# Optimization experiments

Measured on AMD Instinct MI355X. Metric: run time of the kernel, lower is better.

## Reference

```python
import jax, jax.numpy as jnp
import numpy as np

F = 128          # feature_size
N = 512          # num_vertices (batch_size fixed to 1 by the original indexing)
C = 32 * 7 * 7 * 7   # 10976, f2 channel dim
G = 13           # f2 spatial grid (indices = (v+1)*6 in [0,12])
EPS = 1e-5


def _block(x, W1, b1, W2, b2, g, be, m, v):
    # Linear -> ELU -> Linear -> ELU -> Dropout(eval=id) -> BatchNorm1d(eval)
    h = jax.nn.elu(x @ W1 + b1)
    h = jax.nn.elu(h @ W2 + b2)
    return (h - m) * (g * jax.lax.rsqrt(v + EPS)) + be


def setup_inputs() -> dict:
    key = jax.random.key(0)
    ks = iter(jax.random.split(key, 80))

    def nrm(sh, s):
        return jax.random.normal(next(ks), sh, jnp.float32) * s

    def lin(i, o):
        return nrm((i, o), 1.0 / np.sqrt(i)), nrm((o,), 0.01)

    def bn():
        g = 1.0 + nrm((F,), 0.05)
        be = nrm((F,), 0.05)
        m = nrm((F,), 0.1)
        v = jax.random.uniform(next(ks), (F,), jnp.float32) + 0.5
        return g, be, m, v

    d = {}
    d['vertices'] = jax.random.uniform(next(ks), (1, N, 3), jnp.float32) * 2.0 - 1.0
    d['f2'] = nrm((1, G, G, G, C), 0.1)
    ii = jnp.arange(N, dtype=jnp.int32)
    d['v1s_idx'] = jnp.repeat(ii, N)   # edge k=(i,j): i = k//N
    d['v2s_idx'] = jnp.tile(ii, N)     #               j = k%N
    d['adj'] = (jax.random.uniform(next(ks), (N, N)) < 0.05).astype(jnp.float32)

    for p, (i, o) in [('mv', (3, F)), ('mf', (C, F)), ('s1', (2 * F, F)),
                      ('s2', (F, F)), ('s3', (2 * F, F))]:
        W1, b1 = lin(i, o)
        W2, b2 = lin(F, F)
        g, be, m, v = bn()
        d.update({p + '_W1': W1, p + '_b1': b1, p + '_W2': W2, p + '_b2': b2,
                  p + '_g': g, p + '_be': be, p + '_m': m, p + '_v': v})
    W3, b3 = lin(F, 2)
    d['s3_W3'], d['s3_b3'] = W3, b3
    return d


def _forward(vertices, f2, adj,
             mv_W1, mv_b1, mv_W2, mv_b2, mv_g, mv_be, mv_m, mv_v,
             mf_W1, mf_b1, mf_W2, mf_b2, mf_g, mf_be, mf_m, mf_v,
             s1_W1, s1_b1, s1_W2, s1_b2, s1_g, s1_be, s1_m, s1_v,
             s2_W1, s2_b1, s2_W2, s2_b2, s2_g, s2_be, s2_m, s2_v,
             s3_W1, s3_b1, s3_W2, s3_b2, s3_g, s3_be, s3_m, s3_v, s3_W3, s3_b3,
             v1s_idx, v2s_idx):
    b, n, _ = vertices.shape
    flat = vertices.reshape(-1, 3)                        # (B*N, 3)
    idx = ((flat + 1.0) * 6.0).astype(jnp.int32)          # grid indices in [0,12]
    f2e = f2[0, idx[:, 0], idx[:, 1], idx[:, 2], :]       # gather: (B*N, C)
    vf = _block(flat, mv_W1, mv_b1, mv_W2, mv_b2, mv_g, mv_be, mv_m, mv_v)
    ff = _block(f2e, mf_W1, mf_b1, mf_W2, mf_b2, mf_g, mf_be, mf_m, mf_v)
    vert = jnp.concatenate([vf, ff], -1).reshape(b, n, 2 * F)  # (B, N, 2F)

    # stage1: NodeToEdge (endpoint combine) -> MLP block over all N^2 edges
    e1 = vert[:, v1s_idx] + vert[:, v2s_idx]              # (B, N*N, 2F)
    s1 = _block(e1, s1_W1, s1_b1, s1_W2, s1_b2, s1_g, s1_be, s1_m, s1_v)  # (B, E, F)

    # stage2: EdgeToNode (adjacency-masked sum) -> MLP -> NodeToEdge
    nodes = jnp.einsum('bijf,ij->bif', s1.reshape(b, n, n, F), adj)  # (B, N, F)
    n2 = _block(nodes, s2_W1, s2_b1, s2_W2, s2_b2, s2_g, s2_be, s2_m, s2_v)
    s2 = n2[:, v1s_idx] + n2[:, v2s_idx]                  # (B, E, F)

    cat = jnp.concatenate([s1, s2], -1).reshape(b * n * n, 2 * F)
    h = _block(cat, s3_W1, s3_b1, s3_W2, s3_b2, s3_g, s3_be, s3_m, s3_v)
    return (h @ s3_W3 + s3_b3).reshape(b, n, n, 2)


def reference(vertices, f2, v1s_idx, v2s_idx, adj,
              mv_W1, mv_b1, mv_W2, mv_b2, mv_g, mv_be, mv_m, mv_v,
              mf_W1, mf_b1, mf_W2, mf_b2, mf_g, mf_be, mf_m, mf_v,
              s1_W1, s1_b1, s1_W2, s1_b2, s1_g, s1_be, s1_m, s1_v,
              s2_W1, s2_b1, s2_W2, s2_b2, s2_g, s2_be, s2_m, s2_v,
              s3_W1, s3_b1, s3_W2, s3_b2, s3_g, s3_be, s3_m, s3_v, s3_W3, s3_b3):
    return _forward(vertices, f2, adj,
                    mv_W1, mv_b1, mv_W2, mv_b2, mv_g, mv_be, mv_m, mv_v,
                    mf_W1, mf_b1, mf_W2, mf_b2, mf_g, mf_be, mf_m, mf_v,
                    s1_W1, s1_b1, s1_W2, s1_b2, s1_g, s1_be, s1_m, s1_v,
                    s2_W1, s2_b1, s2_W2, s2_b2, s2_g, s2_be, s2_m, s2_v,
                    s3_W1, s3_b1, s3_W2, s3_b2, s3_g, s3_be, s3_m, s3_v, s3_W3, s3_b3,
                    v1s_idx, v2s_idx)
```

## Files before the change

### kernel.cpp

```cpp
#include <hip/hip_runtime.h>
#include <hip/hip_bf16.h>


#define F    128
#define NV   512
#define CCC  10976
#define EPSV 1e-5f

typedef __attribute__((ext_vector_type(8)))  short        short8;
typedef __attribute__((ext_vector_type(4)))  float        f32x4;
typedef __attribute__((ext_vector_type(4)))  float        flt4;
typedef __attribute__((ext_vector_type(4)))  unsigned int u32x4;

union Frag { u32x4 q; short8 s; unsigned int d[4]; unsigned short u[8]; };

__device__ __forceinline__ unsigned short f2bf(float x){
  union { float f; unsigned int u; } c; c.f = x;
  unsigned int r = c.u + 0x7FFFu + ((c.u >> 16) & 1u);
  return (unsigned short)(r >> 16);
}
__device__ __forceinline__ unsigned int pkbf(float a, float b){
  union { __hip_bfloat162 h; unsigned int u; } cv;
  cv.h = __float22bfloat162_rn(make_float2(a, b));
  return cv.u;
}
__device__ __forceinline__ float eluf(float x){
  return x > 0.f ? x : (__expf(x) - 1.f);
}
__device__ __forceinline__ f32x4 mfma16(short8 a, short8 b, f32x4 c){
  return __builtin_amdgcn_mfma_f32_16x16x32_bf16(a, b, c, 0, 0, 0);
}

#define WS_U      0u
#define WS_FFPRE  262144u
#define WS_NODES  524288u
#define WS_WPERM  786432u
#define WS_ADJS   1048576u
#define WS_CNT    1050624u
#define WS_PJ     1052672u
#define WS_VEC    1183744u
#define WS_W2FS1  1188864u
#define WS_W1AFS3 1221632u
#define WS_W2FS3  1254400u
#define WS_W3F    1287168u
#define WS_MFW1F  1291264u
#define WS_END    4101120u
#define WS_PART   4101120u
#define WS_PART_END 8295424u


__global__ __launch_bounds__(256) void k_prep(
    const float* s1W2, const float* s3W1, const float* s3W2, const float* s3W3,
    const float* s1g, const float* s1be, const float* s1m, const float* s1v,
    const float* s3g, const float* s3be, const float* s3m, const float* s3v,
    const float* s1b2, const float* s3b2,
    unsigned short* w2fs1, unsigned short* w1afs3, unsigned short* w2fs3,
    unsigned short* w3f, float* vec, float* zeroreg)
{
  int t = blockIdx.x * 256 + threadIdx.x;
  if (t < 49152){
    int T = t >> 14, tt = t & 16383;
    int e = tt & 7, lane = (tt >> 3) & 63, grp = tt >> 9;
    int slot = (grp >> 3) * 32 + ((lane >> 4) & 3) * 8 + e;
    int col  = (grp & 7) * 16 + (lane & 15);
    float val;
    unsigned short* dst;
    if (T == 0){ dst = w2fs1; val = s1W2[slot * F + col]; }
    else {
      int kf = (slot & 7) * 16 + (slot >> 3);
      if (T == 1){
        float sc1 = s1g[kf] * rsqrtf(s1v[kf] + EPSV);
        dst = w1afs3; val = sc1 * s3W1[kf * F + col];
      } else {
        dst = w2fs3; val = s3W2[kf * F + col];
      }
    }
    dst[tt] = f2bf(val);
    return;
  }
  t -= 49152;
  if (t < 2048){
    int e = t & 7, lane = (t >> 3) & 63, ks = t >> 9;
    int slot = ks * 32 + ((lane >> 4) & 3) * 8 + e;
    int kf = (slot & 7) * 16 + (slot >> 3);
    int n = lane & 15;
    float sc3 = s3g[kf] * rsqrtf(s3v[kf] + EPSV);
    w3f[t] = f2bf(n < 2 ? sc3 * s3W3[kf * 2 + n] : 0.f);
    return;
  }
  t -= 2048;
  if (t < 1024){
    int f = t & 127, which = t >> 7;
    int s = (f & 15) * 8 + (f >> 4);
    switch (which){
      case 0: vec[512 + s] = s1b2[f]; break;
      case 1: vec[640 + s] = s3b2[f]; break;
      case 2: vec[768 + f] = s1g[f] * rsqrtf(s1v[f] + EPSV); break;
      case 3: vec[896 + f] = s1be[f] - s1m[f] * (s1g[f] * rsqrtf(s1v[f] + EPSV)); break;
      case 4: {
        float a = 0.f;
        for (int k = 0; k < F; ++k){
          float sc = s1g[k] * rsqrtf(s1v[k] + EPSV);
          a = fmaf(s1be[k] - s1m[k] * sc, s3W1[k * F + f], a);
        }
        vec[1024 + f] = a;
      } break;
      case 5: if (f < 16){
        float a = 0.f;
        if (f < 2){
          for (int k = 0; k < F; ++k){
            float sc = s3g[k] * rsqrtf(s3v[k] + EPSV);
            a = fmaf(s3be[k] - s3m[k] * sc, s3W3[k * 2 + f], a);
          }
        }
        vec[1152 + f] = a;
      } break;
      default: break;
    }
    return;
  }
  t -= 1024;
  if (t < 65536) zeroreg[t] = 0.f;
}

__global__ __launch_bounds__(256) void k_prepf(
    const float* __restrict__ mfW1, unsigned short* __restrict__ mfw1f)
{
  __shared__ float sm[32 * 132];
  int tid = threadIdx.x, ksg = blockIdx.x;
  const float* src = mfW1 + ksg * 32 * F;
  #pragma unroll
  for (int p = 0; p < 4; ++p){
    int g4 = tid + p * 256;
    int row = g4 >> 5, col = (g4 & 31) * 4;
    flt4 v = *(const flt4*)(src + row * F + col);
    *(flt4*)(sm + row * 132 + col) = v;
  }
  __syncthreads();
  unsigned int* dst = (unsigned int*)mfw1f + ksg * 2048;
  #pragma unroll
  for (int q2 = 0; q2 < 8; ++q2){
    int o = (tid * 8 + q2) * 2;
    int nt = o >> 9, lane = (o >> 3) & 63, e = o & 7;
    int k = (lane >> 4) * 8 + e;
    int n = nt * 16 + (lane & 15);
    dst[tid * 8 + q2] = pkbf(sm[k * 132 + n], sm[(k + 1) * 132 + n]);
  }
}

__global__ __launch_bounds__(256) void k_adj(
    const float* __restrict__ adj, unsigned short* __restrict__ pj,
    int* __restrict__ cntI, float* __restrict__ cntF)
{
  __shared__ unsigned long long msk[8];
  int i = blockIdx.x, tid = threadIdx.x, wv = tid >> 6, ln = tid & 63;
  bool p0 = adj[i * NV + tid] != 0.f;
  bool p1 = adj[i * NV + 256 + tid] != 0.f;
  unsigned long long m0 = __ballot(p0);
  unsigned long long m1 = __ballot(p1);
  if (ln == 0){ msk[wv] = m0; msk[4 + wv] = m1; }
  __syncthreads();
  int base0 = 0, base1 = 0, tot = 0;
  #pragma unroll
  for (int g = 0; g < 8; ++g){
    int c = __popcll(msk[g]);
    if (g < wv) base0 += c;
    if (g < 4 + wv) base1 += c;
    tot += c;
  }
  unsigned long long below = (1ull << ln) - 1ull;
  if (p0){
    int r = base0 + __popcll(m0 & below);
    if (r < 128) pj[i * 128 + r] = (unsigned short)tid;
  }
  if (p1){
    int r = base1 + __popcll(m1 & below);
    if (r < 128) pj[i * 128 + r] = (unsigned short)(256 + tid);
  }
  if (tid == 0){ cntI[i] = tot > 128 ? 128 : tot; cntF[i] = (float)tot; }
}

__global__ __launch_bounds__(256) void k_ff1(
    const float* __restrict__ verts, const float* __restrict__ f2,
    const unsigned short* __restrict__ mfw1f, float* __restrict__ ffpre,
    float* __restrict__ partials, int use_parts)
{
  int tid = threadIdx.x, w = tid >> 6, l = tid & 63, g = l >> 4, mm = l & 15;
  int mb = blockIdx.x & 7, kc = blockIdx.x >> 3;
  int v = mb * 64 + w * 16 + mm;
  float x0 = verts[v * 3 + 0], x1 = verts[v * 3 + 1], x2 = verts[v * 3 + 2];
  int i0 = (int)((x0 + 1.f) * 6.f), i1 = (int)((x1 + 1.f) * 6.f), i2 = (int)((x2 + 1.f) * 6.f);
  int base = ((i0 * 13 + i1) * 13 + i2) * CCC;

  f32x4 zero = {0.f, 0.f, 0.f, 0.f};
  f32x4 acc[8];
  #pragma unroll
  for (int nt = 0; nt < 8; ++nt) acc[nt] = zero;

  const u32x4* bt = (const u32x4*)mfw1f;
  for (int kk = 0; kk < 22; ++kk){
    int ksg = kc * 22 + kk;
    if (ksg >= 343) break;
    const float* ap = f2 + base + ksg * 32 + g * 8;
    flt4 a0 = *(const flt4*)ap;
    flt4 a1 = *(const flt4*)(ap + 4);
    Frag a;
    a.d[0] = pkbf(a0.x, a0.y); a.d[1] = pkbf(a0.z, a0.w);
    a.d[2] = pkbf(a1.x, a1.y); a.d[3] = pkbf(a1.z, a1.w);
    #pragma unroll
    for (int nt = 0; nt < 8; ++nt){
      Frag b; b.q = bt[(ksg * 8 + nt) * 64 + l];
      acc[nt] = mfma16(a.s, b.s, acc[nt]);
    }
  }
  if (use_parts){
    #pragma unroll
    for (int nt = 0; nt < 8; ++nt){
      int n = nt * 16 + mm;
      #pragma unroll
      for (int r = 0; r < 4; ++r)
        partials[(kc * NV + mb * 64 + w * 16 + g * 4 + r) * F + n] = acc[nt][r];
    }
  } else {
    #pragma unroll
    for (int nt = 0; nt < 8; ++nt){
      int n = nt * 16 + mm;
      #pragma unroll
      for (int r = 0; r < 4; ++r)
        atomicAdd(&ffpre[(mb * 64 + w * 16 + g * 4 + r) * F + n], acc[nt][r]);
    }
  }
}

__global__ __launch_bounds__(128) void k_vert(
    const float* __restrict__ verts, const float* __restrict__ ffpre,
    const float* __restrict__ partials, int use_parts,
    const float* mvW1, const float* mvb1, const float* mvW2, const float* mvb2,
    const float* mvg, const float* mvbe, const float* mvm, const float* mvv,
    const float* mfb1, const float* mfW2, const float* mfb2,
    const float* mfg, const float* mfbe, const float* mfm, const float* mfv,
    const float* s1W1, const float* s1b1, float* __restrict__ uP)
{
  __shared__ float hv[F], hf[F], vf[F], ff[F];
  int f = threadIdx.x, v = blockIdx.x;
  float x0 = verts[v * 3], x1 = verts[v * 3 + 1], x2 = verts[v * 3 + 2];
  hv[f] = eluf(mvb1[f] + x0 * mvW1[f] + x1 * mvW1[F + f] + x2 * mvW1[2 * F + f]);
  float fp;
  if (use_parts){
    fp = 0.f;
    for (int kc = 0; kc < 16; ++kc) fp += partials[(kc * NV + v) * F + f];
  } else {
    fp = ffpre[v * F + f];
  }
  hf[f] = eluf(fp + mfb1[f]);
  __syncthreads();
  float sv = mvb2[f], sf = mfb2[f];
  for (int k = 0; k < F; ++k){
    sv = fmaf(hv[k], mvW2[k * F + f], sv);
    sf = fmaf(hf[k], mfW2[k * F + f], sf);
  }
  vf[f] = (eluf(sv) - mvm[f]) * (mvg[f] * rsqrtf(mvv[f] + EPSV)) + mvbe[f];
  ff[f] = (eluf(sf) - mfm[f]) * (mfg[f] * rsqrtf(mfv[f] + EPSV)) + mfbe[f];
  __syncthreads();
  float u = 0.5f * s1b1[f];
  for (int k = 0; k < F; ++k){
    u = fmaf(vf[k], s1W1[k * F + f], u);
    u = fmaf(ff[k], s1W1[(128 + k) * F + f], u);
  }
  uP[v * F + f] = u;
}

__global__ __launch_bounds__(256) void k_pass1s(
    const float* __restrict__ uP, const unsigned short* __restrict__ w2fs1,
    const float* __restrict__ vec, const unsigned short* __restrict__ pj,
    const int* __restrict__ cntA, float* __restrict__ nodes)
{
  __shared__ u32x4 Wb[2048];
  __shared__ float ci[F], nblk[F];
  int tid = threadIdx.x, i = blockIdx.x;
  int cnt = cntA[i];
  { const u32x4* ws_ = (const u32x4*)w2fs1;
    #pragma unroll
    for (int ii = 0; ii < 8; ++ii) Wb[tid + 256 * ii] = ws_[tid + 256 * ii]; }
  if (tid < F){ ci[tid] = uP[i * F + tid]; nblk[tid] = 0.f; }
  __syncthreads();

  int w = tid >> 6, l = tid & 63, g = l >> 4, mm = l & 15;
  float b2v[8];
  *(flt4*)&b2v[0] = *(const flt4*)(vec + 512 + mm * 8);
  *(flt4*)&b2v[4] = *(const flt4*)(vec + 516 + mm * 8);

  for (int t = 0; t * 64 < cnt; ++t){
    int row = t * 64 + w * 16 + mm;
    int j = (row < cnt) ? (int)pj[i * 128 + row] : 0;
    f32x4 acc[8];
    #pragma unroll
    for (int nt = 0; nt < 8; ++nt){ float b = b2v[nt]; acc[nt] = (f32x4){b, b, b, b}; }
    #pragma unroll
    for (int ks = 0; ks < 4; ++ks){
      int kb = ks * 32 + g * 8;
      flt4 ua = *(const flt4*)(uP + j * F + kb);
      flt4 ub = *(const flt4*)(uP + j * F + kb + 4);
      flt4 c0 = *(const flt4*)&ci[kb];
      flt4 c1 = *(const flt4*)&ci[kb + 4];
      Frag a;
      a.d[0] = pkbf(eluf(ua.x + c0.x), eluf(ua.y + c0.y));
      a.d[1] = pkbf(eluf(ua.z + c0.z), eluf(ua.w + c0.w));
      a.d[2] = pkbf(eluf(ub.x + c1.x), eluf(ub.y + c1.y));
      a.d[3] = pkbf(eluf(ub.z + c1.z), eluf(ub.w + c1.w));
      #pragma unroll
      for (int nt = 0; nt < 8; ++nt){
        Frag b; b.q = Wb[(ks * 8 + nt) * 64 + l];
        acc[nt] = mfma16(a.s, b.s, acc[nt]);
      }
    }
    int rbase = t * 64 + w * 16 + g * 4;
    float mk[4];
    #pragma unroll
    for (int r = 0; r < 4; ++r) mk[r] = (rbase + r < cnt) ? 1.f : 0.f;
    #pragma unroll
    for (int nt = 0; nt < 8; ++nt){
      float s = mk[0] * eluf(acc[nt][0]);
      s = fmaf(mk[1], eluf(acc[nt][1]), s);
      s = fmaf(mk[2], eluf(acc[nt][2]), s);
      s = fmaf(mk[3], eluf(acc[nt][3]), s);
      s += __shfl_xor(s, 16, 64);
      s += __shfl_xor(s, 32, 64);
      if (l < 16) atomicAdd(&nblk[nt * 16 + mm], s);
    }
  }
  __syncthreads();
  if (tid < F) nodes[i * F + tid] = nblk[tid];
}

__global__ __launch_bounds__(128) void k_mid(
    const float* __restrict__ nodes, const float* __restrict__ cntF,
    const float* __restrict__ vec,
    const float* s2W1, const float* s2b1, const float* s2W2, const float* s2b2,
    const float* s2g, const float* s2be, const float* s2m, const float* s2v,
    const float* s3W1, const float* s3b1, float* __restrict__ wPp)
{
  __shared__ float a[F], b[F];
  int f = threadIdx.x, r = blockIdx.x;
  a[f] = vec[768 + f] * nodes[r * F + f] + vec[896 + f] * cntF[r];
  __syncthreads();
  float s = s2b1[f];
  for (int k = 0; k < F; ++k) s = fmaf(a[k], s2W1[k * F + f], s);
  b[f] = eluf(s);
  __syncthreads();
  float s2 = s2b2[f];
  for (int k = 0; k < F; ++k) s2 = fmaf(b[k], s2W2[k * F + f], s2);
  float n2 = (eluf(s2) - s2m[f]) * (s2g[f] * rsqrtf(s2v[f] + EPSV)) + s2be[f];
  __syncthreads();
  a[f] = n2;
  __syncthreads();
  float wv = 0.5f * (s3b1[f] + vec[1024 + f]);
  for (int k = 0; k < F; ++k) wv = fmaf(a[k], s3W1[(128 + k) * F + f], wv);
  wPp[r * F + ((f & 15) * 8 + (f >> 4))] = wv;
}

__global__ __launch_bounds__(512, 4) void k_pass3(
    const float* __restrict__ uP, const float* __restrict__ wPp,
    const unsigned short* __restrict__ w2fs1, const unsigned short* __restrict__ w1afs3,
    const unsigned short* __restrict__ w2fs3, const unsigned short* __restrict__ w3f,
    const float* __restrict__ vec, const float* __restrict__ s3b3,
    float* __restrict__ out)
{
  __shared__ u32x4 Wb[2048];
  __shared__ __align__(16) char Hb[32768];
  __shared__ float ci[F];
  int tid = threadIdx.x, bid = blockIdx.x;
  int band, idx;
  if (bid < 512)      { band = 0; idx = bid; }
  else if (bid < 896) { band = 1; idx = bid - 512; }
  else if (bid < 1152){ band = 2; idx = bid - 896; }
  else                { band = 3; idx = bid - 1152; }
  int tpb = 4 - band;
  int i  = band * 128 + idx / tpb;
  int j0 = (band + idx % tpb) * 128;

  int w = tid >> 6, l = tid & 63, g = l >> 4, mm = l & 15;
  char* hb = Hb + w * 4096;

  { const u32x4* ws_ = (const u32x4*)w2fs1;
    #pragma unroll
    for (int ii = 0; ii < 4; ++ii) Wb[tid + 512 * ii] = ws_[tid + 512 * ii]; }
  if (tid < F) ci[tid] = uP[i * F + tid];
  __syncthreads();

  int j = j0 + w * 16 + mm;
  f32x4 acc[8];
  {
    float b2v[8];
    *(flt4*)&b2v[0] = *(const flt4*)(vec + 512 + mm * 8);
    *(flt4*)&b2v[4] = *(const flt4*)(vec + 516 + mm * 8);
    #pragma unroll
    for (int nt = 0; nt < 8; ++nt){ float b = b2v[nt]; acc[nt] = (f32x4){b, b, b, b}; }
  }
  #pragma unroll
  for (int ks = 0; ks < 4; ++ks){
    int kb = ks * 32 + g * 8;
    flt4 ua = *(const flt4*)(uP + j * F + kb);
    flt4 ub = *(const flt4*)(uP + j * F + kb + 4);
    flt4 c0 = *(const flt4*)&ci[kb];
    flt4 c1 = *(const flt4*)&ci[kb + 4];
    Frag a;
    a.d[0] = pkbf(eluf(ua.x + c0.x), eluf(ua.y + c0.y));
    a.d[1] = pkbf(eluf(ua.z + c0.z), eluf(ua.w + c0.w));
    a.d[2] = pkbf(eluf(ub.x + c1.x), eluf(ub.y + c1.y));
    a.d[3] = pkbf(eluf(ub.z + c1.z), eluf(ub.w + c1.w));
    #pragma unroll
    for (int nt = 0; nt < 8; ++nt){
      Frag b; b.q = Wb[(ks * 8 + nt) * 64 + l];
      acc[nt] = mfma16(a.s, b.s, acc[nt]);
    }
  }
  #pragma unroll
  for (int r = 0; r < 4; ++r){
    int row = g * 4 + r;
    u32x4 wd;
    #pragma unroll
    for (int q = 0; q < 4; ++q)
      wd[q] = pkbf(eluf(acc[2*q][r]), eluf(acc[2*q+1][r]));
    *(u32x4*)(hb + row * 256 + ((mm * 16) ^ ((row & 7) << 4))) = wd;
  }
  __syncthreads();
  { const u32x4* ws_ = (const u32x4*)w1afs3;
    #pragma unroll
    for (int ii = 0; ii < 4; ++ii) Wb[tid + 512 * ii] = ws_[tid + 512 * ii]; }
  __syncthreads();

  {
    float wiv[8];
    *(flt4*)&wiv[0] = *(const flt4*)(wPp + i * F + mm * 8);
    *(flt4*)&wiv[4] = *(const flt4*)(wPp + i * F + mm * 8 + 4);
    #pragma unroll
    for (int nt = 0; nt < 8; ++nt){ float b = wiv[nt]; acc[nt] = (f32x4){b, b, b, b}; }
  }
  {
    int sx = (mm & 7) << 4;
    #pragma unroll
    for (int ks = 0; ks < 4; ++ks){
      Frag a; a.q = *(const u32x4*)(hb + mm * 256 + ((ks * 64 + g * 16) ^ sx));
      #pragma unroll
      for (int nt = 0; nt < 8; ++nt){
        Frag b; b.q = Wb[(ks * 8 + nt) * 64 + l];
        acc[nt] = mfma16(a.s, b.s, acc[nt]);
      }
    }
  }
  #pragma unroll
  for (int r = 0; r < 4; ++r){
    int row = g * 4 + r;
    int jj = j0 + w * 16 + row;
    float wjv[8];
    *(flt4*)&wjv[0] = *(const flt4*)(wPp + jj * F + mm * 8);
    *(flt4*)&wjv[4] = *(const flt4*)(wPp + jj * F + mm * 8 + 4);
    u32x4 wd;
    #pragma unroll
    for (int q = 0; q < 4; ++q)
      wd[q] = pkbf(eluf(acc[2*q][r] + wjv[2*q]), eluf(acc[2*q+1][r] + wjv[2*q+1]));
    *(u32x4*)(hb + row * 256 + ((mm * 16) ^ ((row & 7) << 4))) = wd;
  }
  __syncthreads();
  { const u32x4* ws_ = (const u32x4*)w2fs3;
    #pragma unroll
    for (int ii = 0; ii < 4; ++ii) Wb[tid + 512 * ii] = ws_[tid + 512 * ii]; }
  __syncthreads();

  {
    float b2v[8];
    *(flt4*)&b2v[0] = *(const flt4*)(vec + 640 + mm * 8);
    *(flt4*)&b2v[4] = *(const flt4*)(vec + 644 + mm * 8);
    #pragma unroll
    for (int nt = 0; nt < 8; ++nt){ float b = b2v[nt]; acc[nt] = (f32x4){b, b, b, b}; }
  }
  {
    int sx = (mm & 7) << 4;
    #pragma unroll
    for (int ks = 0; ks < 4; ++ks){
      Frag a; a.q = *(const u32x4*)(hb + mm * 256 + ((ks * 64 + g * 16) ^ sx));
      #pragma unroll
      for (int nt = 0; nt < 8; ++nt){
        Frag b; b.q = Wb[(ks * 8 + nt) * 64 + l];
        acc[nt] = mfma16(a.s, b.s, acc[nt]);
      }
    }
  }
  #pragma unroll
  for (int r = 0; r < 4; ++r){
    int row = g * 4 + r;
    u32x4 wd;
    #pragma unroll
    for (int q = 0; q < 4; ++q)
      wd[q] = pkbf(eluf(acc[2*q][r]), eluf(acc[2*q+1][r]));
    *(u32x4*)(hb + row * 256 + ((mm * 16) ^ ((row & 7) << 4))) = wd;
  }

  float bb = (mm < 2) ? (s3b3[mm] + vec[1152 + mm]) : 0.f;
  f32x4 acc4 = {bb, bb, bb, bb};
  {
    const u32x4* w3q = (const u32x4*)w3f;
    int sx = (mm & 7) << 4;
    #pragma unroll
    for (int ks = 0; ks < 4; ++ks){
      Frag a; a.q = *(const u32x4*)(hb + mm * 256 + ((ks * 64 + g * 16) ^ sx));
      Frag b; b.q = w3q[ks * 64 + l];
      acc4 = mfma16(a.s, b.s, acc4);
    }
  }
  if (mm < 2){
    #pragma unroll
    for (int r = 0; r < 4; ++r){
      int jr = j0 + w * 16 + g * 4 + r;
      if (jr >= i){
        float val = acc4[r];
        out[(i * NV + jr) * 2 + mm] = val;
        out[(jr * NV + i) * 2 + mm] = val;
      }
    }
  }
}

extern "C" void kernel_launch(void* const* d_in, const int* in_sizes, int n_in,
                              void* d_out, int out_size, void* d_ws, size_t ws_size,
                              hipStream_t stream)
{
  (void)in_sizes; (void)n_in; (void)out_size;
  const float* vertices = (const float*)d_in[0];
  const float* f2   = (const float*)d_in[1];
  const float* adj  = (const float*)d_in[4];
  const float* mvW1 = (const float*)d_in[5];
  const float* mvb1 = (const float*)d_in[6];
  const float* mvW2 = (const float*)d_in[7];
  const float* mvb2 = (const float*)d_in[8];
  const float* mvg  = (const float*)d_in[9];
  const float* mvbe = (const float*)d_in[10];
  const float* mvm  = (const float*)d_in[11];
  const float* mvv  = (const float*)d_in[12];
  const float* mfW1 = (const float*)d_in[13];
  const float* mfb1 = (const float*)d_in[14];
  const float* mfW2 = (const float*)d_in[15];
  const float* mfb2 = (const float*)d_in[16];
  const float* mfg  = (const float*)d_in[17];
  const float* mfbe = (const float*)d_in[18];
  const float* mfm  = (const float*)d_in[19];
  const float* mfv  = (const float*)d_in[20];
  const float* s1W1 = (const float*)d_in[21];
  const float* s1b1 = (const float*)d_in[22];
  const float* s1W2 = (const float*)d_in[23];
  const float* s1b2 = (const float*)d_in[24];
  const float* s1g  = (const float*)d_in[25];
  const float* s1be = (const float*)d_in[26];
  const float* s1m  = (const float*)d_in[27];
  const float* s1v  = (const float*)d_in[28];
  const float* s2W1 = (const float*)d_in[29];
  const float* s2b1 = (const float*)d_in[30];
  const float* s2W2 = (const float*)d_in[31];
  const float* s2b2 = (const float*)d_in[32];
  const float* s2g  = (const float*)d_in[33];
  const float* s2be = (const float*)d_in[34];
  const float* s2m  = (const float*)d_in[35];
  const float* s2v  = (const float*)d_in[36];
  const float* s3W1 = (const float*)d_in[37];
  const float* s3b1 = (const float*)d_in[38];
  const float* s3W2 = (const float*)d_in[39];
  const float* s3b2 = (const float*)d_in[40];
  const float* s3g  = (const float*)d_in[41];
  const float* s3be = (const float*)d_in[42];
  const float* s3m  = (const float*)d_in[43];
  const float* s3v  = (const float*)d_in[44];
  const float* s3W3 = (const float*)d_in[45];
  const float* s3b3 = (const float*)d_in[46];

  char* ws = (char*)d_ws;
  float* uP    = (float*)(ws + WS_U);
  float* ffpre = (float*)(ws + WS_FFPRE);
  float* nodes = (float*)(ws + WS_NODES);
  float* wPp   = (float*)(ws + WS_WPERM);
  float* cntF  = (float*)(ws + WS_ADJS);
  int*   cntI  = (int*)(ws + WS_CNT);
  unsigned short* pj = (unsigned short*)(ws + WS_PJ);
  float* vec   = (float*)(ws + WS_VEC);
  unsigned short* w2fs1  = (unsigned short*)(ws + WS_W2FS1);
  unsigned short* w1afs3 = (unsigned short*)(ws + WS_W1AFS3);
  unsigned short* w2fs3  = (unsigned short*)(ws + WS_W2FS3);
  unsigned short* w3f    = (unsigned short*)(ws + WS_W3F);
  unsigned short* mfw1f  = (unsigned short*)(ws + WS_MFW1F);
  float* parts = (float*)(ws + WS_PART);
  int use_parts = (ws_size >= (size_t)WS_PART_END) ? 1 : 0;

  k_prep<<<460, 256, 0, stream>>>(s1W2, s3W1, s3W2, s3W3,
      s1g, s1be, s1m, s1v, s3g, s3be, s3m, s3v, s1b2, s3b2,
      w2fs1, w1afs3, w2fs3, w3f, vec, ffpre);
  k_prepf<<<343, 256, 0, stream>>>(mfW1, mfw1f);
  k_adj<<<512, 256, 0, stream>>>(adj, pj, cntI, cntF);
  k_ff1<<<128, 256, 0, stream>>>(vertices, f2, mfw1f, ffpre, parts, use_parts);
  k_vert<<<512, 128, 0, stream>>>(vertices, ffpre, parts, use_parts,
      mvW1, mvb1, mvW2, mvb2, mvg, mvbe, mvm, mvv,
      mfb1, mfW2, mfb2, mfg, mfbe, mfm, mfv,
      s1W1, s1b1, uP);
  k_pass1s<<<512, 256, 0, stream>>>(uP, w2fs1, vec, pj, cntI, nodes);
  k_mid<<<512, 128, 0, stream>>>(nodes, cntF, vec,
      s2W1, s2b1, s2W2, s2b2, s2g, s2be, s2m, s2v, s3W1, s3b1, wPp);
  k_pass3<<<1280, 512, 0, stream>>>(uP, wPp, w2fs1, w1afs3, w2fs3, w3f, vec,
      s3b3, (float*)d_out);
}
```

Baseline: 114.9 us.

## Merge prep kernels, split ff1 K-range finer, and double rows per wave in pass3

```diff
diff --git a/kernel.cpp b/kernel.cpp
--- a/kernel.cpp
+++ b/kernel.cpp
@@ -46,138 +46,143 @@
 #define WS_MFW1F  1291264u
 #define WS_END    4101120u
 #define WS_PART   4101120u
-#define WS_PART_END 8295424u
-
-
-__global__ __launch_bounds__(256) void k_prep(
+#define WS_PART_END 15373312u
+
+
+__global__ __launch_bounds__(256) void k_setup(
     const float* s1W2, const float* s3W1, const float* s3W2, const float* s3W3,
+    const float* __restrict__ mfW1,
     const float* s1g, const float* s1be, const float* s1m, const float* s1v,
     const float* s3g, const float* s3be, const float* s3m, const float* s3v,
-    const float* s1b2, const float* s3b2,
+    const float* s1b2, const float* s3b2, const float* __restrict__ adj,
     unsigned short* w2fs1, unsigned short* w1afs3, unsigned short* w2fs3,
-    unsigned short* w3f, float* vec, float* zeroreg)
-{
-  int t = blockIdx.x * 256 + threadIdx.x;
-  if (t < 49152){
-    int T = t >> 14, tt = t & 16383;
-    int e = tt & 7, lane = (tt >> 3) & 63, grp = tt >> 9;
-    int slot = (grp >> 3) * 32 + ((lane >> 4) & 3) * 8 + e;
-    int col  = (grp & 7) * 16 + (lane & 15);
-    float val;
-    unsigned short* dst;
-    if (T == 0){ dst = w2fs1; val = s1W2[slot * F + col]; }
-    else {
-      int kf = (slot & 7) * 16 + (slot >> 3);
-      if (T == 1){
-        float sc1 = s1g[kf] * rsqrtf(s1v[kf] + EPSV);
-        dst = w1afs3; val = sc1 * s3W1[kf * F + col];
-      } else {
-        dst = w2fs3; val = s3W2[kf * F + col];
-      }
-    }
-    dst[tt] = f2bf(val);
-    return;
-  }
-  t -= 49152;
-  if (t < 2048){
-    int e = t & 7, lane = (t >> 3) & 63, ks = t >> 9;
-    int slot = ks * 32 + ((lane >> 4) & 3) * 8 + e;
-    int kf = (slot & 7) * 16 + (slot >> 3);
-    int n = lane & 15;
-    float sc3 = s3g[kf] * rsqrtf(s3v[kf] + EPSV);
-    w3f[t] = f2bf(n < 2 ? sc3 * s3W3[kf * 2 + n] : 0.f);
-    return;
-  }
-  t -= 2048;
-  if (t < 1024){
-    int f = t & 127, which = t >> 7;
-    int s = (f & 15) * 8 + (f >> 4);
-    switch (which){
-      case 0: vec[512 + s] = s1b2[f]; break;
-      case 1: vec[640 + s] = s3b2[f]; break;
-      case 2: vec[768 + f] = s1g[f] * rsqrtf(s1v[f] + EPSV); break;
-      case 3: vec[896 + f] = s1be[f] - s1m[f] * (s1g[f] * rsqrtf(s1v[f] + EPSV)); break;
-      case 4: {
-        float a = 0.f;
-        for (int k = 0; k < F; ++k){
-          float sc = s1g[k] * rsqrtf(s1v[k] + EPSV);
-          a = fmaf(s1be[k] - s1m[k] * sc, s3W1[k * F + f], a);
-        }
-        vec[1024 + f] = a;
-      } break;
-      case 5: if (f < 16){
-        float a = 0.f;
-        if (f < 2){
-          for (int k = 0; k < F; ++k){
-            float sc = s3g[k] * rsqrtf(s3v[k] + EPSV);
-            a = fmaf(s3be[k] - s3m[k] * sc, s3W3[k * 2 + f], a);
-          }
-        }
-        vec[1152 + f] = a;
-      } break;
-      default: break;
-    }
-    return;
-  }
-  t -= 1024;
-  if (t < 65536) zeroreg[t] = 0.f;
-}
-
-__global__ __launch_bounds__(256) void k_prepf(
-    const float* __restrict__ mfW1, unsigned short* __restrict__ mfw1f)
+    unsigned short* w3f, unsigned short* __restrict__ mfw1f,
+    float* vec, float* zeroreg,
+    unsigned short* __restrict__ pj, int* __restrict__ cntI,
+    float* __restrict__ cntF)
 {
   __shared__ float sm[32 * 132];
-  int tid = threadIdx.x, ksg = blockIdx.x;
-  const float* src = mfW1 + ksg * 32 * F;
-  #pragma unroll
-  for (int p = 0; p < 4; ++p){
-    int g4 = tid + p * 256;
-    int row = g4 >> 5, col = (g4 & 31) * 4;
-    flt4 v = *(const flt4*)(src + row * F + col);
-    *(flt4*)(sm + row * 132 + col) = v;
-  }
-  __syncthreads();
-  unsigned int* dst = (unsigned int*)mfw1f + ksg * 2048;
-  #pragma unroll
-  for (int q2 = 0; q2 < 8; ++q2){
-    int o = (tid * 8 + q2) * 2;
-    int nt = o >> 9, lane = (o >> 3) & 63, e = o & 7;
-    int k = (lane >> 4) * 8 + e;
-    int n = nt * 16 + (lane & 15);
-    dst[tid * 8 + q2] = pkbf(sm[k * 132 + n], sm[(k + 1) * 132 + n]);
-  }
-}
-
-__global__ __launch_bounds__(256) void k_adj(
-    const float* __restrict__ adj, unsigned short* __restrict__ pj,
-    int* __restrict__ cntI, float* __restrict__ cntF)
-{
   __shared__ unsigned long long msk[8];
-  int i = blockIdx.x, tid = threadIdx.x, wv = tid >> 6, ln = tid & 63;
-  bool p0 = adj[i * NV + tid] != 0.f;
-  bool p1 = adj[i * NV + 256 + tid] != 0.f;
-  unsigned long long m0 = __ballot(p0);
-  unsigned long long m1 = __ballot(p1);
-  if (ln == 0){ msk[wv] = m0; msk[4 + wv] = m1; }
-  __syncthreads();
-  int base0 = 0, base1 = 0, tot = 0;
-  #pragma unroll
-  for (int g = 0; g < 8; ++g){
-    int c = __popcll(msk[g]);
-    if (g < wv) base0 += c;
-    if (g < 4 + wv) base1 += c;
-    tot += c;
-  }
-  unsigned long long below = (1ull << ln) - 1ull;
-  if (p0){
-    int r = base0 + __popcll(m0 & below);
-    if (r < 128) pj[i * 128 + r] = (unsigned short)tid;
-  }
-  if (p1){
-    int r = base1 + __popcll(m1 & below);
-    if (r < 128) pj[i * 128 + r] = (unsigned short)(256 + tid);
-  }
-  if (tid == 0){ cntI[i] = tot > 128 ? 128 : tot; cntF[i] = (float)tot; }
+  int bid = blockIdx.x, tid = threadIdx.x;
+
+  if (bid < 460){
+    int t = bid * 256 + tid;
+    if (t < 49152){
+      int T = t >> 14, tt = t & 16383;
+      int e = tt & 7, lane = (tt >> 3) & 63, grp = tt >> 9;
+      int slot = (grp >> 3) * 32 + ((lane >> 4) & 3) * 8 + e;
+      int col  = (grp & 7) * 16 + (lane & 15);
+      float val;
+      unsigned short* dst;
+      if (T == 0){ dst = w2fs1; val = s1W2[slot * F + col]; }
+      else {
+        int kf = (slot & 7) * 16 + (slot >> 3);
+        if (T == 1){
+          float sc1 = s1g[kf] * rsqrtf(s1v[kf] + EPSV);
+          dst = w1afs3; val = sc1 * s3W1[kf * F + col];
+        } else {
+          dst = w2fs3; val = s3W2[kf * F + col];
+        }
+      }
+      dst[tt] = f2bf(val);
+      return;
+    }
+    t -= 49152;
+    if (t < 2048){
+      int e = t & 7, lane = (t >> 3) & 63, ks = t >> 9;
+      int slot = ks * 32 + ((lane >> 4) & 3) * 8 + e;
+      int kf = (slot & 7) * 16 + (slot >> 3);
+      int n = lane & 15;
+      float sc3 = s3g[kf] * rsqrtf(s3v[kf] + EPSV);
+      w3f[t] = f2bf(n < 2 ? sc3 * s3W3[kf * 2 + n] : 0.f);
+      return;
+    }
+    t -= 2048;
+    if (t < 1024){
+      int f = t & 127, which = t >> 7;
+      int s = (f & 15) * 8 + (f >> 4);
+      switch (which){
+        case 0: vec[512 + s] = s1b2[f]; break;
+        case 1: vec[640 + s] = s3b2[f]; break;
+        case 2: vec[768 + f] = s1g[f] * rsqrtf(s1v[f] + EPSV); break;
+        case 3: vec[896 + f] = s1be[f] - s1m[f] * (s1g[f] * rsqrtf(s1v[f] + EPSV)); break;
+        case 4: {
+          float a = 0.f;
+          for (int k = 0; k < F; ++k){
+            float sc = s1g[k] * rsqrtf(s1v[k] + EPSV);
+            a = fmaf(s1be[k] - s1m[k] * sc, s3W1[k * F + f], a);
+          }
+          vec[1024 + f] = a;
+        } break;
+        case 5: if (f < 16){
+          float a = 0.f;
+          if (f < 2){
+            for (int k = 0; k < F; ++k){
+              float sc = s3g[k] * rsqrtf(s3v[k] + EPSV);
+              a = fmaf(s3be[k] - s3m[k] * sc, s3W3[k * 2 + f], a);
+            }
+          }
+          vec[1152 + f] = a;
+        } break;
+        default: break;
+      }
+      return;
+    }
+    t -= 1024;
+    if (t < 65536) zeroreg[t] = 0.f;
+    return;
+  }
+
+  if (bid < 803){
+    int ksg = bid - 460;
+    const float* src = mfW1 + ksg * 32 * F;
+    #pragma unroll
+    for (int p = 0; p < 4; ++p){
+      int g4 = tid + p * 256;
+      int row = g4 >> 5, col = (g4 & 31) * 4;
+      flt4 v = *(const flt4*)(src + row * F + col);
+      *(flt4*)(sm + row * 132 + col) = v;
+    }
+    __syncthreads();
+    unsigned int* dst = (unsigned int*)mfw1f + ksg * 2048;
+    #pragma unroll
+    for (int q2 = 0; q2 < 8; ++q2){
+      int o = (tid * 8 + q2) * 2;
+      int nt = o >> 9, lane = (o >> 3) & 63, e = o & 7;
+      int k = (lane >> 4) * 8 + e;
+      int n = nt * 16 + (lane & 15);
+      dst[tid * 8 + q2] = pkbf(sm[k * 132 + n], sm[(k + 1) * 132 + n]);
+    }
+    return;
+  }
+
+  {
+    int i = bid - 803, wv = tid >> 6, ln = tid & 63;
+    bool p0 = adj[i * NV + tid] != 0.f;
+    bool p1 = adj[i * NV + 256 + tid] != 0.f;
+    unsigned long long m0 = __ballot(p0);
+    unsigned long long m1 = __ballot(p1);
+    if (ln == 0){ msk[wv] = m0; msk[4 + wv] = m1; }
+    __syncthreads();
+    int base0 = 0, base1 = 0, tot = 0;
+    #pragma unroll
+    for (int g = 0; g < 8; ++g){
+      int c = __popcll(msk[g]);
+      if (g < wv) base0 += c;
+      if (g < 4 + wv) base1 += c;
+      tot += c;
+    }
+    unsigned long long below = (1ull << ln) - 1ull;
+    if (p0){
+      int r = base0 + __popcll(m0 & below);
+      if (r < 128) pj[i * 128 + r] = (unsigned short)tid;
+    }
+    if (p1){
+      int r = base1 + __popcll(m1 & below);
+      if (r < 128) pj[i * 128 + r] = (unsigned short)(256 + tid);
+    }
+    if (tid == 0){ cntI[i] = tot > 128 ? 128 : tot; cntF[i] = (float)tot; }
+  }
 }
 
 __global__ __launch_bounds__(256) void k_ff1(
@@ -198,8 +203,9 @@
   for (int nt = 0; nt < 8; ++nt) acc[nt] = zero;
 
   const u32x4* bt = (const u32x4*)mfw1f;
-  for (int kk = 0; kk < 22; ++kk){
-    int ksg = kc * 22 + kk;
+  #pragma unroll
+  for (int kk = 0; kk < 8; ++kk){
+    int ksg = kc * 8 + kk;
     if (ksg >= 343) break;
     const float* ap = f2 + base + ksg * 32 + g * 8;
     flt4 a0 = *(const flt4*)ap;
@@ -248,7 +254,7 @@
   float fp;
   if (use_parts){
     fp = 0.f;
-    for (int kc = 0; kc < 16; ++kc) fp += partials[(kc * NV + v) * F + f];
+    for (int kc = 0; kc < 43; ++kc) fp += partials[(kc * NV + v) * F + f];
   } else {
     fp = ffpre[v * F + f];
   }
@@ -359,7 +365,7 @@
   wPp[r * F + ((f & 15) * 8 + (f >> 4))] = wv;
 }
 
-__global__ __launch_bounds__(512, 4) void k_pass3(
+__global__ __launch_bounds__(256, 2) void k_pass3(
     const float* __restrict__ uP, const float* __restrict__ wPp,
     const unsigned short* __restrict__ w2fs1, const unsigned short* __restrict__ w1afs3,
     const unsigned short* __restrict__ w2fs3, const unsigned short* __restrict__ w3f,
@@ -380,54 +386,70 @@
   int j0 = (band + idx % tpb) * 128;
 
   int w = tid >> 6, l = tid & 63, g = l >> 4, mm = l & 15;
-  char* hb = Hb + w * 4096;
+  char* hb = Hb + w * 8192;
+  int jbase = j0 + w * 32;
+  int sx = (mm & 7) << 4;
 
   { const u32x4* ws_ = (const u32x4*)w2fs1;
     #pragma unroll
-    for (int ii = 0; ii < 4; ++ii) Wb[tid + 512 * ii] = ws_[tid + 512 * ii]; }
+    for (int ii = 0; ii < 8; ++ii) Wb[tid + 256 * ii] = ws_[tid + 256 * ii]; }
   if (tid < F) ci[tid] = uP[i * F + tid];
   __syncthreads();
 
-  int j = j0 + w * 16 + mm;
-  f32x4 acc[8];
+  f32x4 acc[2][8];
   {
     float b2v[8];
     *(flt4*)&b2v[0] = *(const flt4*)(vec + 512 + mm * 8);
     *(flt4*)&b2v[4] = *(const flt4*)(vec + 516 + mm * 8);
     #pragma unroll
-    for (int nt = 0; nt < 8; ++nt){ float b = b2v[nt]; acc[nt] = (f32x4){b, b, b, b}; }
+    for (int m = 0; m < 2; ++m)
+    #pragma unroll
+    for (int nt = 0; nt < 8; ++nt){ float b = b2v[nt]; acc[m][nt] = (f32x4){b, b, b, b}; }
   }
   #pragma unroll
   for (int ks = 0; ks < 4; ++ks){
     int kb = ks * 32 + g * 8;
-    flt4 ua = *(const flt4*)(uP + j * F + kb);
-    flt4 ub = *(const flt4*)(uP + j * F + kb + 4);
     flt4 c0 = *(const flt4*)&ci[kb];
     flt4 c1 = *(const flt4*)&ci[kb + 4];
-    Frag a;
-    a.d[0] = pkbf(eluf(ua.x + c0.x), eluf(ua.y + c0.y));
-    a.d[1] = pkbf(eluf(ua.z + c0.z), eluf(ua.w + c0.w));
-    a.d[2] = pkbf(eluf(ub.x + c1.x), eluf(ub.y + c1.y));
-    a.d[3] = pkbf(eluf(ub.z + c1.z), eluf(ub.w + c1.w));
+    Frag a0, a1;
+    {
+      const float* p0 = uP + (jbase + mm) * F + kb;
+      flt4 ua = *(const flt4*)p0;
+      flt4 ub = *(const flt4*)(p0 + 4);
+      a0.d[0] = pkbf(eluf(ua.x + c0.x), eluf(ua.y + c0.y));
+      a0.d[1] = pkbf(eluf(ua.z + c0.z), eluf(ua.w + c0.w));
+      a0.d[2] = pkbf(eluf(ub.x + c1.x), eluf(ub.y + c1.y));
+      a0.d[3] = pkbf(eluf(ub.z + c1.z), eluf(ub.w + c1.w));
+      const float* p1 = uP + (jbase + 16 + mm) * F + kb;
+      flt4 va = *(const flt4*)p1;
+      flt4 vb = *(const flt4*)(p1 + 4);
+      a1.d[0] = pkbf(eluf(va.x + c0.x), eluf(va.y + c0.y));
+      a1.d[1] = pkbf(eluf(va.z + c0.z), eluf(va.w + c0.w));
+      a1.d[2] = pkbf(eluf(vb.x + c1.x), eluf(vb.y + c1.y));
+      a1.d[3] = pkbf(eluf(vb.z + c1.z), eluf(vb.w + c1.w));
+    }
     #pragma unroll
     for (int nt = 0; nt < 8; ++nt){
       Frag b; b.q = Wb[(ks * 8 + nt) * 64 + l];
-      acc[nt] = mfma16(a.s, b.s, acc[nt]);
-    }
-  }
+      acc[0][nt] = mfma16(a0.s, b.s, acc[0][nt]);
+      acc[1][nt] = mfma16(a1.s, b.s, acc[1][nt]);
+    }
+  }
+  #pragma unroll
+  for (int m = 0; m < 2; ++m)
   #pragma unroll
   for (int r = 0; r < 4; ++r){
-    int row = g * 4 + r;
+    int row = m * 16 + g * 4 + r;
     u32x4 wd;
     #pragma unroll
     for (int q = 0; q < 4; ++q)
-      wd[q] = pkbf(eluf(acc[2*q][r]), eluf(acc[2*q+1][r]));
+      wd[q] = pkbf(eluf(acc[m][2*q][r]), eluf(acc[m][2*q+1][r]));
     *(u32x4*)(hb + row * 256 + ((mm * 16) ^ ((row & 7) << 4))) = wd;
   }
   __syncthreads();
   { const u32x4* ws_ = (const u32x4*)w1afs3;
     #pragma unroll
-    for (int ii = 0; ii < 4; ++ii) Wb[tid + 512 * ii] = ws_[tid + 512 * ii]; }
+    for (int ii = 0; ii < 8; ++ii) Wb[tid + 256 * ii] = ws_[tid + 256 * ii]; }
   __syncthreads();
 
   {
@@ -435,37 +457,40 @@
     *(flt4*)&wiv[0] = *(const flt4*)(wPp + i * F + mm * 8);
     *(flt4*)&wiv[4] = *(const flt4*)(wPp + i * F + mm * 8 + 4);
     #pragma unroll
-    for (int nt = 0; nt < 8; ++nt){ float b = wiv[nt]; acc[nt] = (f32x4){b, b, b, b}; }
-  }
-  {
-    int sx = (mm & 7) << 4;
-    #pragma unroll
-    for (int ks = 0; ks < 4; ++ks){
-      Frag a; a.q = *(const u32x4*)(hb + mm * 256 + ((ks * 64 + g * 16) ^ sx));
-      #pragma unroll
-      for (int nt = 0; nt < 8; ++nt){
-        Frag b; b.q = Wb[(ks * 8 + nt) * 64 + l];
-        acc[nt] = mfma16(a.s, b.s, acc[nt]);
-      }
-    }
-  }
+    for (int m = 0; m < 2; ++m)
+    #pragma unroll
+    for (int nt = 0; nt < 8; ++nt){ float b = wiv[nt]; acc[m][nt] = (f32x4){b, b, b, b}; }
+  }
+  #pragma unroll
+  for (int ks = 0; ks < 4; ++ks){
+    Frag a0; a0.q = *(const u32x4*)(hb + mm * 256 + ((ks * 64 + g * 16) ^ sx));
+    Frag a1; a1.q = *(const u32x4*)(hb + (16 + mm) * 256 + ((ks * 64 + g * 16) ^ sx));
+    #pragma unroll
+    for (int nt = 0; nt < 8; ++nt){
+      Frag b; b.q = Wb[(ks * 8 + nt) * 64 + l];
+      acc[0][nt] = mfma16(a0.s, b.s, acc[0][nt]);
+      acc[1][nt] = mfma16(a1.s, b.s, acc[1][nt]);
+    }
+  }
+  #pragma unroll
+  for (int m = 0; m < 2; ++m)
   #pragma unroll
   for (int r = 0; r < 4; ++r){
-    int row = g * 4 + r;
-    int jj = j0 + w * 16 + row;
+    int row = m * 16 + g * 4 + r;
+    int jj = jbase + row;
     float wjv[8];
     *(flt4*)&wjv[0] = *(const flt4*)(wPp + jj * F + mm * 8);
     *(flt4*)&wjv[4] = *(const flt4*)(wPp + jj * F + mm * 8 + 4);
     u32x4 wd;
     #pragma unroll
     for (int q = 0; q < 4; ++q)
-      wd[q] = pkbf(eluf(acc[2*q][r] + wjv[2*q]), eluf(acc[2*q+1][r] + wjv[2*q+1]));
+      wd[q] = pkbf(eluf(acc[m][2*q][r] + wjv[2*q]), eluf(acc[m][2*q+1][r] + wjv[2*q+1]));
     *(u32x4*)(hb + row * 256 + ((mm * 16) ^ ((row & 7) << 4))) = wd;
   }
   __syncthreads();
   { const u32x4* ws_ = (const u32x4*)w2fs3;
     #pragma unroll
-    for (int ii = 0; ii < 4; ++ii) Wb[tid + 512 * ii] = ws_[tid + 512 * ii]; }
+    for (int ii = 0; ii < 8; ++ii) Wb[tid + 256 * ii] = ws_[tid + 256 * ii]; }
   __syncthreads();
 
   {
@@ -473,48 +498,54 @@
     *(flt4*)&b2v[0] = *(const flt4*)(vec + 640 + mm * 8);
     *(flt4*)&b2v[4] = *(const flt4*)(vec + 644 + mm * 8);
     #pragma unroll
-    for (int nt = 0; nt < 8; ++nt){ float b = b2v[nt]; acc[nt] = (f32x4){b, b, b, b}; }
-  }
-  {
-    int sx = (mm & 7) << 4;
-    #pragma unroll
-    for (int ks = 0; ks < 4; ++ks){
-      Frag a; a.q = *(const u32x4*)(hb + mm * 256 + ((ks * 64 + g * 16) ^ sx));
-      #pragma unroll
-      for (int nt = 0; nt < 8; ++nt){
-        Frag b; b.q = Wb[(ks * 8 + nt) * 64 + l];
-        acc[nt] = mfma16(a.s, b.s, acc[nt]);
-      }
-    }
-  }
+    for (int m = 0; m < 2; ++m)
+    #pragma unroll
+    for (int nt = 0; nt < 8; ++nt){ float b = b2v[nt]; acc[m][nt] = (f32x4){b, b, b, b}; }
+  }
+  #pragma unroll
+  for (int ks = 0; ks < 4; ++ks){
+    Frag a0; a0.q = *(const u32x4*)(hb + mm * 256 + ((ks * 64 + g * 16) ^ sx));
+    Frag a1; a1.q = *(const u32x4*)(hb + (16 + mm) * 256 + ((ks * 64 + g * 16) ^ sx));
+    #pragma unroll
+    for (int nt = 0; nt < 8; ++nt){
+      Frag b; b.q = Wb[(ks * 8 + nt) * 64 + l];
+      acc[0][nt] = mfma16(a0.s, b.s, acc[0][nt]);
+      acc[1][nt] = mfma16(a1.s, b.s, acc[1][nt]);
+    }
+  }
+  #pragma unroll
+  for (int m = 0; m < 2; ++m)
   #pragma unroll
   for (int r = 0; r < 4; ++r){
-    int row = g * 4 + r;
+    int row = m * 16 + g * 4 + r;
     u32x4 wd;
     #pragma unroll
     for (int q = 0; q < 4; ++q)
-      wd[q] = pkbf(eluf(acc[2*q][r]), eluf(acc[2*q+1][r]));
+      wd[q] = pkbf(eluf(acc[m][2*q][r]), eluf(acc[m][2*q+1][r]));
     *(u32x4*)(hb + row * 256 + ((mm * 16) ^ ((row & 7) << 4))) = wd;
   }
 
   float bb = (mm < 2) ? (s3b3[mm] + vec[1152 + mm]) : 0.f;
-  f32x4 acc4 = {bb, bb, bb, bb};
+  f32x4 acc4[2] = {{bb, bb, bb, bb}, {bb, bb, bb, bb}};
   {
     const u32x4* w3q = (const u32x4*)w3f;
-    int sx = (mm & 7) << 4;
     #pragma unroll
     for (int ks = 0; ks < 4; ++ks){
-      Frag a; a.q = *(const u32x4*)(hb + mm * 256 + ((ks * 64 + g * 16) ^ sx));
+      Frag a0; a0.q = *(const u32x4*)(hb + mm * 256 + ((ks * 64 + g * 16) ^ sx));
+      Frag a1; a1.q = *(const u32x4*)(hb + (16 + mm) * 256 + ((ks * 64 + g * 16) ^ sx));
       Frag b; b.q = w3q[ks * 64 + l];
-      acc4 = mfma16(a.s, b.s, acc4);
+      acc4[0] = mfma16(a0.s, b.s, acc4[0]);
+      acc4[1] = mfma16(a1.s, b.s, acc4[1]);
     }
   }
   if (mm < 2){
     #pragma unroll
+    for (int m = 0; m < 2; ++m)
+    #pragma unroll
     for (int r = 0; r < 4; ++r){
-      int jr = j0 + w * 16 + g * 4 + r;
+      int jr = jbase + m * 16 + g * 4 + r;
       if (jr >= i){
-        float val = acc4[r];
+        float val = acc4[m][r];
         out[(i * NV + jr) * 2 + mm] = val;
         out[(jr * NV + i) * 2 + mm] = val;
       }
@@ -590,12 +621,10 @@
   float* parts = (float*)(ws + WS_PART);
   int use_parts = (ws_size >= (size_t)WS_PART_END) ? 1 : 0;
 
-  k_prep<<<460, 256, 0, stream>>>(s1W2, s3W1, s3W2, s3W3,
-      s1g, s1be, s1m, s1v, s3g, s3be, s3m, s3v, s1b2, s3b2,
-      w2fs1, w1afs3, w2fs3, w3f, vec, ffpre);
-  k_prepf<<<343, 256, 0, stream>>>(mfW1, mfw1f);
-  k_adj<<<512, 256, 0, stream>>>(adj, pj, cntI, cntF);
-  k_ff1<<<128, 256, 0, stream>>>(vertices, f2, mfw1f, ffpre, parts, use_parts);
+  k_setup<<<1315, 256, 0, stream>>>(s1W2, s3W1, s3W2, s3W3, mfW1,
+      s1g, s1be, s1m, s1v, s3g, s3be, s3m, s3v, s1b2, s3b2, adj,
+      w2fs1, w1afs3, w2fs3, w3f, mfw1f, vec, ffpre, pj, cntI, cntF);
+  k_ff1<<<344, 256, 0, stream>>>(vertices, f2, mfw1f, ffpre, parts, use_parts);
   k_vert<<<512, 128, 0, stream>>>(vertices, ffpre, parts, use_parts,
       mvW1, mvb1, mvW2, mvb2, mvg, mvbe, mvm, mvv,
       mfb1, mfW2, mfb2, mfg, mfbe, mfm, mfv,
@@ -603,6 +632,6 @@
   k_pass1s<<<512, 256, 0, stream>>>(uP, w2fs1, vec, pj, cntI, nodes);
   k_mid<<<512, 128, 0, stream>>>(nodes, cntF, vec,
       s2W1, s2b1, s2W2, s2b2, s2g, s2be, s2m, s2v, s3W1, s3b1, wPp);
-  k_pass3<<<1280, 512, 0, stream>>>(uP, wPp, w2fs1, w1afs3, w2fs3, w3f, vec,
+  k_pass3<<<1280, 256, 0, stream>>>(uP, wPp, w2fs1, w1afs3, w2fs3, w3f, vec,
       s3b3, (float*)d_out);
 }
```

After: 109.6 us. 4.6% less time.
